# Kernel tuning notes

Hardware: AMD Instinct MI355X
Metric: run time of the kernel (lower is better)

## Reference

```python
import jax, jax.numpy as jnp
import numpy as np

N, FIN, H, FOUT = 4096, 128, 4, 64
NEG_INF = -1e9


def _xavier(key, shape):
    fan_in, fan_out = shape[-2], shape[-1]
    limit = float(np.sqrt(6.0 / (fan_in + fan_out)))
    return jax.random.uniform(key, shape, jnp.float32, -limit, limit)


def setup_inputs() -> dict:
    key = jax.random.key(0)
    ks = jax.random.split(key, 7)
    x = jax.random.normal(ks[0], (N, FIN), jnp.float32)
    u = jax.random.uniform(ks[1], (N, N))
    mask = jnp.where(u < 0.02, 0.0, NEG_INF).astype(jnp.float32)
    idx = jnp.arange(N)
    mask = mask.at[idx, idx].set(0.0)
    proj_param = _xavier(ks[2], (H, FIN, FOUT))          # per-head projection
    score_src = _xavier(ks[3], (H, FOUT, 1))             # scoring_fn_source (IMP1 layout)
    score_tgt = _xavier(ks[4], (H, FOUT, 1))             # scoring_fn_target
    skip_w = _xavier(ks[5], (H * FOUT, FIN))             # skip_proj Linear weight
    bias = jnp.zeros((H * FOUT,), jnp.float32)
    return {"x": x, "mask": mask, "proj_param": proj_param,
            "score_src": score_src, "score_tgt": score_tgt,
            "skip_w": skip_w, "bias": bias}


def reference(x, mask, proj_param, score_src, score_tgt, skip_w, bias):
    # project: [1,N,Fin] @ [H,Fin,Fout] -> [H,N,Fout]
    h = jnp.einsum('nf,hfo->hno', x, proj_param)
    # additive (Bahdanau-style) scores
    s_src = jnp.matmul(h, score_src)                     # [H,N,1]
    s_tgt = jnp.matmul(h, score_tgt)                     # [H,N,1]
    all_scores = jax.nn.leaky_relu(s_src + jnp.swapaxes(s_tgt, 1, 2), 0.2)  # [H,N,N]
    attn = jax.nn.softmax(all_scores + mask[None, :, :], axis=-1)           # [H,N,N]
    # aggregate: [H,N,N] @ [H,N,Fout] -> [N,H,Fout]
    out = jnp.einsum('hnm,hmo->nho', attn, h)
    # skip connection (dims differ: Fin != H*Fout -> use skip_proj)
    out = out + jnp.matmul(x, skip_w.T).reshape(N, H, FOUT)
    out = out.reshape(N, H * FOUT) + bias                # concat heads + bias
    return jax.nn.elu(out)
```

## Files before the change

kernel.cpp:

```cpp
#include <hip/hip_runtime.h>
#include <hip/hip_bf16.h>
#include <math.h>


#define NN   4096
#define FIN  128
#define NH   4
#define FO   64
#define HF   256
#define SEG  96
#define LIST 192
#define GEMM_BLOCKS 512

typedef unsigned short ushort_t;
typedef unsigned int uint4n __attribute__((ext_vector_type(4)));

__device__ __forceinline__ ushort_t f2bf(float f) {
    __hip_bfloat16 h = __float2bfloat16(f);
    union { __hip_bfloat16 h; ushort_t u; } c; c.h = h; return c.u;
}
__device__ __forceinline__ float bf2f(ushort_t u) {
    union { unsigned int i; float f; } c; c.i = ((unsigned int)u) << 16; return c.f;
}

__global__ __launch_bounds__(256) void k0_fused(
        const float* __restrict__ x,
        const float* __restrict__ proj,
        const float* __restrict__ skw,
        const float* __restrict__ asrc,
        const float* __restrict__ atgt,
        const unsigned int* __restrict__ mask,
        ushort_t* __restrict__ h2b, float* __restrict__ skip_ws,
        float* __restrict__ src4, float* __restrict__ tgt4,
        ushort_t* __restrict__ list, int* __restrict__ cnt) {
    __shared__ float sA[64 * 68];
    __shared__ float sB[64 * 64];
    const int tid = threadIdx.x;
    const int blk = blockIdx.x;

    if (blk >= GEMM_BLOCKS) {
        const int i    = blk - GEMM_BLOCKS;
        ushort_t* s_nbr = (ushort_t*)sA;
        int*      s_wt  = (int*)sB;
        const int lane = tid & 63, w = tid >> 6;

        const uint4n* mrow = (const uint4n*)(mask + (size_t)i * NN);
        uint4n mv[4];
        #pragma unroll
        for (int s = 0; s < 4; s++)
            mv[s] = __builtin_nontemporal_load(&mrow[w * 256 + s * 64 + lane]);

        int base = 0;
        #pragma unroll
        for (int s = 0; s < 4; s++) {
            #pragma unroll
            for (int e = 0; e < 4; e++) {
                bool hit = (mv[s][e] & 0x7fffffffu) == 0u;
                unsigned long long bal = __ballot(hit);
                int pre = __builtin_amdgcn_mbcnt_hi(
                              (unsigned int)(bal >> 32),
                              __builtin_amdgcn_mbcnt_lo((unsigned int)bal, 0));
                if (hit) {
                    int slot = base + pre;
                    if (slot < SEG)
                        s_nbr[w * SEG + slot] =
                            (ushort_t)(w * 1024 + s * 256 + lane * 4 + e);
                }
                base += (int)__popcll(bal);
            }
        }
        if (lane == 0) s_wt[w] = base < SEG ? base : SEG;
        __syncthreads();

        const int t0 = s_wt[0], t1 = s_wt[1], t2 = s_wt[2], t3 = s_wt[3];
        const int off = (w > 0 ? t0 : 0) + (w > 1 ? t1 : 0) + (w > 2 ? t2 : 0);
        const int mine = s_wt[w];
        ushort_t* dst = list + (size_t)i * LIST;
        for (int kk = lane; kk < mine; kk += 64) {
            int p = off + kk;
            if (p < LIST) dst[p] = s_nbr[w * SEG + kk];
        }
        if (tid == 0) {
            int tot = t0 + t1 + t2 + t3;
            cnt[i] = tot < LIST ? tot : LIST;
        }
        return;
    }

    const int bc = blk >> 6;
    const int i0 = (blk & 63) * 64;
    const int tx = tid & 15, ty = tid >> 4;
    const int r0 = ty << 2, c0 = tx << 2;
    float acc[4][4] = {};

    #pragma unroll
    for (int kb = 0; kb < FIN; kb += 64) {
        if (kb) __syncthreads();
        #pragma unroll
        for (int q = 0; q < 4; q++) {
            int s   = tid + q * 256;
            int row = s >> 4;
            int c4  = (s & 15) << 2;
            float4 v = *(const float4*)(x + (size_t)(i0 + row) * FIN + kb + c4);
            float* d = sA + row * 68 + c4;
            d[0] = v.x; d[1] = v.y; d[2] = v.z; d[3] = v.w;
        }
        if (bc < 4) {
            const float4* src = (const float4*)(proj + (size_t)bc * FIN * FO
                                                + (size_t)kb * FO);
            #pragma unroll
            for (int q = 0; q < 4; q++) {
                int s = tid + q * 256;
                *(float4*)(sB + (size_t)s * 4) = src[s];
            }
        } else {
            const float* sw = skw + (size_t)(bc - 4) * 64 * FIN;
            #pragma unroll
            for (int q = 0; q < 4; q++) {
                int s  = tid + q * 256;
                int c  = s & 63;
                int k4 = (s >> 6) << 2;
                float4 v = *(const float4*)(sw + (size_t)c * FIN + kb + k4);
                sB[(k4 + 0) * 64 + c] = v.x;
                sB[(k4 + 1) * 64 + c] = v.y;
                sB[(k4 + 2) * 64 + c] = v.z;
                sB[(k4 + 3) * 64 + c] = v.w;
            }
        }
        __syncthreads();

        #pragma unroll 2
        for (int k = 0; k < 64; k += 4) {
            alignas(16) float a[4][4];
            alignas(16) float b[4][4];
            #pragma unroll
            for (int rr = 0; rr < 4; rr++)
                *(float4*)a[rr] = *(const float4*)(sA + (r0 + rr) * 68 + k);
            #pragma unroll
            for (int kk = 0; kk < 4; kk++)
                *(float4*)b[kk] = *(const float4*)(sB + (k + kk) * 64 + c0);
            #pragma unroll
            for (int kk = 0; kk < 4; kk++)
                #pragma unroll
                for (int rr = 0; rr < 4; rr++)
                    #pragma unroll
                    for (int cc = 0; cc < 4; cc++)
                        acc[rr][cc] = fmaf(a[rr][kk], b[kk][cc], acc[rr][cc]);
        }
    }

    if (bc < 4) {
        #pragma unroll
        for (int rr = 0; rr < 4; rr++) {
            ushort4 hv;
            hv.x = f2bf(acc[rr][0]); hv.y = f2bf(acc[rr][1]);
            hv.z = f2bf(acc[rr][2]); hv.w = f2bf(acc[rr][3]);
            *(ushort4*)(h2b + (size_t)(i0 + r0 + rr) * HF + bc * 64 + c0) = hv;
        }
        float as[4], at[4];
        #pragma unroll
        for (int cc = 0; cc < 4; cc++) {
            as[cc] = asrc[bc * FO + c0 + cc];
            at[cc] = atgt[bc * FO + c0 + cc];
        }
        #pragma unroll
        for (int rr = 0; rr < 4; rr++) {
            float ps = acc[rr][0] * as[0] + acc[rr][1] * as[1]
                     + acc[rr][2] * as[2] + acc[rr][3] * as[3];
            float pt = acc[rr][0] * at[0] + acc[rr][1] * at[1]
                     + acc[rr][2] * at[2] + acc[rr][3] * at[3];
            #pragma unroll
            for (int off = 8; off >= 1; off >>= 1) {
                ps += __shfl_xor(ps, off, 64);
                pt += __shfl_xor(pt, off, 64);
            }
            if (tx == 0) {
                int i = i0 + r0 + rr;
                src4[(size_t)i * 4 + bc] = ps;
                tgt4[(size_t)i * 4 + bc] = pt;
            }
        }
    } else {
        float* dst = skip_ws + (size_t)i0 * HF + (bc - 4) * 64;
        #pragma unroll
        for (int rr = 0; rr < 4; rr++)
            *(float4*)(dst + (size_t)(r0 + rr) * HF + c0) = *(float4*)acc[rr];
    }
}

__global__ __launch_bounds__(256) void k2b_attn(
        const ushort_t* __restrict__ list,
        const int* __restrict__ cnt,
        const ushort_t* __restrict__ h2b,
        const float* __restrict__ skip_ws,
        const float* __restrict__ src4,
        const float* __restrict__ tgt4,
        const float* __restrict__ bias,
        float* __restrict__ out) {
    __shared__ float s_p[4][LIST];
    __shared__ int   s_j[LIST];
    const int tid  = threadIdx.x;
    const int lane = tid & 63, w = tid >> 6;
    const int i    = blockIdx.x;
    const int col  = w * 64 + lane;

    const float skipv = skip_ws[(size_t)i * HF + col];
    const float bv    = bias[col];
    const float sc    = src4[(size_t)i * 4 + w];
    int c = cnt[i];
    c = c < LIST ? c : LIST;

    const ushort_t* lp = list + (size_t)i * LIST;
    for (int kk = tid; kk < c; kk += 256) s_j[kk] = lp[kk];
    __syncthreads();

    float lsum = 0.f;
    for (int kk = lane; kk < c; kk += 64) {
        int j = s_j[kk];
        float p = sc + tgt4[(size_t)j * 4 + w];
        p = p > 0.f ? p : 0.2f * p;
        p = __expf(p);
        s_p[w][kk] = p;
        lsum += p;
    }
    #pragma unroll
    for (int off = 32; off >= 1; off >>= 1)
        lsum += __shfl_xor(lsum, off, 64);
    const float inv = lsum > 0.f ? 1.0f / lsum : 0.0f;

    const ushort_t* hp = h2b + col;
    const float* ps = s_p[w];
    float acc = 0.f;
    int kk = 0;
    for (; kk + 8 <= c; kk += 8) {
        int j0 = s_j[kk + 0], j1 = s_j[kk + 1], j2 = s_j[kk + 2], j3 = s_j[kk + 3];
        int j4 = s_j[kk + 4], j5 = s_j[kk + 5], j6 = s_j[kk + 6], j7 = s_j[kk + 7];
        float p0 = ps[kk + 0], p1 = ps[kk + 1], p2 = ps[kk + 2], p3 = ps[kk + 3];
        float p4 = ps[kk + 4], p5 = ps[kk + 5], p6 = ps[kk + 6], p7 = ps[kk + 7];
        float h0 = bf2f(hp[(size_t)j0 * HF]);
        float h1 = bf2f(hp[(size_t)j1 * HF]);
        float h2v = bf2f(hp[(size_t)j2 * HF]);
        float h3 = bf2f(hp[(size_t)j3 * HF]);
        float h4 = bf2f(hp[(size_t)j4 * HF]);
        float h5 = bf2f(hp[(size_t)j5 * HF]);
        float h6 = bf2f(hp[(size_t)j6 * HF]);
        float h7 = bf2f(hp[(size_t)j7 * HF]);
        acc = fmaf(p0, h0, acc);  acc = fmaf(p1, h1, acc);
        acc = fmaf(p2, h2v, acc); acc = fmaf(p3, h3, acc);
        acc = fmaf(p4, h4, acc);  acc = fmaf(p5, h5, acc);
        acc = fmaf(p6, h6, acc);  acc = fmaf(p7, h7, acc);
    }
    for (; kk < c; kk++)
        acc = fmaf(ps[kk], bf2f(hp[(size_t)s_j[kk] * HF]), acc);

    float vv = acc * inv + skipv + bv;
    vv = vv > 0.f ? vv : expm1f(vv);
    out[(size_t)i * HF + col] = vv;
}

extern "C" void kernel_launch(void* const* d_in, const int* in_sizes, int n_in,
                              void* d_out, int out_size, void* d_ws, size_t ws_size,
                              hipStream_t stream) {
    const float*        x    = (const float*)d_in[0];
    const unsigned int* mask = (const unsigned int*)d_in[1];
    const float*        proj = (const float*)d_in[2];
    const float*        asrc = (const float*)d_in[3];
    const float*        atgt = (const float*)d_in[4];
    const float*        skw  = (const float*)d_in[5];
    const float*        bias = (const float*)d_in[6];
    float*              out  = (float*)d_out;

    char* ws = (char*)d_ws;
    ushort_t* h2b     = (ushort_t*)ws;
    float*    skip_ws = (float*)(ws + (2u << 20));
    float*    src4    = (float*)(ws + (6u << 20));
    float*    tgt4    = (float*)(ws + (6u << 20) + (64u << 10));
    ushort_t* list    = (ushort_t*)(ws + (8u << 20));
    int*      cntp    = (int*)(ws + (10u << 20));

    hipLaunchKernelGGL(k0_fused, dim3(GEMM_BLOCKS + NN), dim3(256), 0, stream,
                       x, proj, skw, asrc, atgt, mask,
                       h2b, skip_ws, src4, tgt4, list, cntp);
    hipLaunchKernelGGL(k2b_attn, dim3(NN), dim3(256), 0, stream,
                       list, cntp, h2b, skip_ws, src4, tgt4, bias, out);
}
```

Baseline: 140.1 us.

## Scan four mask rows per block with next-row register prefetch

The mask-scan part of the fused first kernel now gives each block four consecutive rows instead of one, cutting the scan grid from 4096 to 1024 blocks. While one row is compacted into the neighbour list, the next row's mask data is loaded into registers. The per-warp count buffer is double-buffered so a single barrier per row is enough. The aim is to cut per-block launch overhead and hide load latency on the 64 MB mask read. In exchange the nontemporal load hint is dropped and fewer blocks are in flight.

```diff
diff --git a/kernel.cpp b/kernel.cpp
--- a/kernel.cpp
+++ b/kernel.cpp
@@ -11,6 +11,8 @@
 #define SEG  96
 #define LIST 192
 #define GEMM_BLOCKS 512
+#define SCAN_BLOCKS 1024
+#define ROWS_PER    4
 
 typedef unsigned short ushort_t;
 typedef unsigned int uint4n __attribute__((ext_vector_type(4)));
@@ -39,50 +41,62 @@
     const int blk = blockIdx.x;
 
     if (blk >= GEMM_BLOCKS) {
-        const int i    = blk - GEMM_BLOCKS;
         ushort_t* s_nbr = (ushort_t*)sA;
-        int*      s_wt  = (int*)sB;
+        int (*s_wt)[4]  = (int(*)[4])sB;
         const int lane = tid & 63, w = tid >> 6;
-
-        const uint4n* mrow = (const uint4n*)(mask + (size_t)i * NN);
-        uint4n mv[4];
+        const int row0 = (blk - GEMM_BLOCKS) * ROWS_PER;
+        const uint4n* mb = (const uint4n*)mask;
+        const size_t wl = (size_t)(w * 256 + lane);
+
+        uint4n cur[4], nxt[4];
         #pragma unroll
         for (int s = 0; s < 4; s++)
-            mv[s] = __builtin_nontemporal_load(&mrow[w * 256 + s * 64 + lane]);
-
-        int base = 0;
-        #pragma unroll
-        for (int s = 0; s < 4; s++) {
-            #pragma unroll
-            for (int e = 0; e < 4; e++) {
-                bool hit = (mv[s][e] & 0x7fffffffu) == 0u;
-                unsigned long long bal = __ballot(hit);
-                int pre = __builtin_amdgcn_mbcnt_hi(
-                              (unsigned int)(bal >> 32),
-                              __builtin_amdgcn_mbcnt_lo((unsigned int)bal, 0));
-                if (hit) {
-                    int slot = base + pre;
-                    if (slot < SEG)
-                        s_nbr[w * SEG + slot] =
-                            (ushort_t)(w * 1024 + s * 256 + lane * 4 + e);
+            cur[s] = mb[(size_t)row0 * 1024 + wl + s * 64];
+
+        for (int rr = 0; rr < ROWS_PER; rr++) {
+            const int i = row0 + rr;
+            if (rr + 1 < ROWS_PER) {
+                #pragma unroll
+                for (int s = 0; s < 4; s++)
+                    nxt[s] = mb[(size_t)(i + 1) * 1024 + wl + s * 64];
+            }
+            int base = 0;
+            #pragma unroll
+            for (int s = 0; s < 4; s++) {
+                #pragma unroll
+                for (int e = 0; e < 4; e++) {
+                    bool hit = (cur[s][e] & 0x7fffffffu) == 0u;
+                    unsigned long long bal = __ballot(hit);
+                    int pre = __builtin_amdgcn_mbcnt_hi(
+                                  (unsigned int)(bal >> 32),
+                                  __builtin_amdgcn_mbcnt_lo((unsigned int)bal, 0));
+                    if (hit) {
+                        int slot = base + pre;
+                        if (slot < SEG)
+                            s_nbr[w * SEG + slot] =
+                                (ushort_t)(w * 1024 + s * 256 + lane * 4 + e);
+                    }
+                    base += (int)__popcll(bal);
                 }
-                base += (int)__popcll(bal);
-            }
-        }
-        if (lane == 0) s_wt[w] = base < SEG ? base : SEG;
-        __syncthreads();
-
-        const int t0 = s_wt[0], t1 = s_wt[1], t2 = s_wt[2], t3 = s_wt[3];
-        const int off = (w > 0 ? t0 : 0) + (w > 1 ? t1 : 0) + (w > 2 ? t2 : 0);
-        const int mine = s_wt[w];
-        ushort_t* dst = list + (size_t)i * LIST;
-        for (int kk = lane; kk < mine; kk += 64) {
-            int p = off + kk;
-            if (p < LIST) dst[p] = s_nbr[w * SEG + kk];
-        }
-        if (tid == 0) {
-            int tot = t0 + t1 + t2 + t3;
-            cnt[i] = tot < LIST ? tot : LIST;
+            }
+            const int p = rr & 1;
+            if (lane == 0) s_wt[p][w] = base < SEG ? base : SEG;
+            __syncthreads();
+            const int t0 = s_wt[p][0], t1 = s_wt[p][1],
+                      t2 = s_wt[p][2], t3 = s_wt[p][3];
+            const int off = (w > 0 ? t0 : 0) + (w > 1 ? t1 : 0) + (w > 2 ? t2 : 0);
+            const int mine = s_wt[p][w];
+            ushort_t* dst = list + (size_t)i * LIST;
+            for (int kk = lane; kk < mine; kk += 64) {
+                int pp = off + kk;
+                if (pp < LIST) dst[pp] = s_nbr[w * SEG + kk];
+            }
+            if (tid == 0) {
+                int tot = t0 + t1 + t2 + t3;
+                cnt[i] = tot < LIST ? tot : LIST;
+            }
+            #pragma unroll
+            for (int s = 0; s < 4; s++) cur[s] = nxt[s];
         }
         return;
     }
@@ -278,7 +292,8 @@
     ushort_t* list    = (ushort_t*)(ws + (8u << 20));
     int*      cntp    = (int*)(ws + (10u << 20));
 
-    hipLaunchKernelGGL(k0_fused, dim3(GEMM_BLOCKS + NN), dim3(256), 0, stream,
+    hipLaunchKernelGGL(k0_fused, dim3(GEMM_BLOCKS + SCAN_BLOCKS), dim3(256),
+                       0, stream,
                        x, proj, skw, asrc, atgt, mask,
                        h2b, skip_ws, src4, tgt4, list, cntp);
     hipLaunchKernelGGL(k2b_attn, dim3(NN), dim3(256), 0, stream,
```

After: 133.3 us. -4.9%, faster.
